# Kernel optimization log

Measured on AMD Instinct MI355X. Metric: run time of the kernel, lower is better.

The kernel has to match this reference:

```python
import jax, jax.numpy as jnp
import numpy as np
from jax import lax

D_MODEL = 512; D_FF = 2048
D_STATE = 16; D_CONV = 4; EXPAND = 2          # mamba_ssm defaults
D_INNER = EXPAND * D_MODEL                    # 1024
DT_RANK = (D_MODEL + 15) // 16                # 32
B, W, C, D = 2, 1024, 64, 8                   # C*D == D_MODEL


def setup_inputs():
    key = jax.random.key(0)
    ks = jax.random.split(key, 24)
    def p(k, shape, s=0.02):
        return jax.random.normal(k, shape, jnp.float32) * s
    inp = {"x": jax.random.normal(ks[0], (B, W, C, D), jnp.float32)}
    for i, pref in enumerate(["fm", "bm"]):
        o = 1 + i * 7
        inp[pref + "_in_W"] = p(ks[o], (2 * D_INNER, D_MODEL))
        inp[pref + "_conv_W"] = p(ks[o + 1], (D_INNER, D_CONV))
        inp[pref + "_conv_b"] = jnp.zeros((D_INNER,), jnp.float32)
        inp[pref + "_xproj_W"] = p(ks[o + 2], (DT_RANK + 2 * D_STATE, D_INNER))
        inp[pref + "_dt_W"] = p(ks[o + 3], (D_INNER, DT_RANK))
        inp[pref + "_dt_b"] = p(ks[o + 4], (D_INNER,), 0.1)
        inp[pref + "_A_log"] = jnp.log(jnp.broadcast_to(
            jnp.arange(1, D_STATE + 1, dtype=jnp.float32), (D_INNER, D_STATE)))
        inp[pref + "_D"] = jnp.ones((D_INNER,), jnp.float32)
        inp[pref + "_out_W"] = p(ks[o + 5], (D_MODEL, D_INNER))
    inp["ln1_g"] = jnp.ones((D_MODEL,), jnp.float32); inp["ln1_b"] = jnp.zeros((D_MODEL,), jnp.float32)
    inp["ln2_g"] = jnp.ones((D_MODEL,), jnp.float32); inp["ln2_b"] = jnp.zeros((D_MODEL,), jnp.float32)
    inp["ln3_g"] = jnp.ones((D_MODEL,), jnp.float32); inp["ln3_b"] = jnp.zeros((D_MODEL,), jnp.float32)
    inp["ff_W1"] = p(ks[15], (D_FF, D_MODEL)); inp["ff_b1"] = jnp.zeros((D_FF,), jnp.float32)
    inp["ff_W2"] = p(ks[16], (D_MODEL, D_FF)); inp["ff_b2"] = jnp.zeros((D_MODEL,), jnp.float32)
    return inp


def _silu(x):
    return x * jax.nn.sigmoid(x)


def _layernorm(x, g, b, eps=1e-5):
    mu = jnp.mean(x, -1, keepdims=True)
    var = jnp.var(x, -1, keepdims=True)
    return (x - mu) * lax.rsqrt(var + eps) * g + b


def _mamba(u, in_W, conv_W, conv_b, xproj_W, dt_W, dt_b, A_log, Dp, out_W):
    # u: (B, L, d_model). Standard Mamba block (mamba_ssm reference math).
    xz = jnp.einsum('bld,ed->ble', u, in_W)            # (B, L, 2*d_inner)
    xm, z = jnp.split(xz, 2, axis=-1)
    # causal depthwise conv along L
    xc = lax.conv_general_dilated(
        xm.transpose(0, 2, 1), conv_W[:, None, :], (1,),
        [(D_CONV - 1, 0)], feature_group_count=D_INNER)
    xm = _silu((xc + conv_b[None, :, None]).transpose(0, 2, 1))  # (B, L, d_inner)
    dbc = jnp.einsum('bld,ed->ble', xm, xproj_W)       # (B, L, dt_rank + 2*d_state)
    dt = dbc[..., :DT_RANK]
    Bm = dbc[..., DT_RANK:DT_RANK + D_STATE]           # (B, L, d_state)
    Cm = dbc[..., DT_RANK + D_STATE:]                  # (B, L, d_state)
    delta = jax.nn.softplus(jnp.einsum('blr,dr->bld', dt, dt_W) + dt_b)  # (B, L, d_inner)
    A = -jnp.exp(A_log)                                # (d_inner, d_state)
    dA = jnp.exp(delta[..., None] * A)                 # (B, L, d_inner, d_state)
    dBu = delta[..., None] * Bm[:, :, None, :] * xm[..., None]

    def step(h, inputs):
        dA_t, dBu_t = inputs
        h = dA_t * h + dBu_t
        return h, h

    h0 = jnp.zeros((u.shape[0], D_INNER, D_STATE), u.dtype)
    _, hs = lax.scan(step, h0, (dA.transpose(1, 0, 2, 3), dBu.transpose(1, 0, 2, 3)))
    y = jnp.einsum('lbds,lbs->bld', hs, Cm.transpose(1, 0, 2))
    y = y + xm * Dp
    y = y * _silu(z)
    return jnp.einsum('ble,de->bld', y, out_W)         # (B, L, d_model)


def reference(x,
              fm_in_W, fm_conv_W, fm_conv_b, fm_xproj_W, fm_dt_W, fm_dt_b, fm_A_log, fm_D, fm_out_W,
              bm_in_W, bm_conv_W, bm_conv_b, bm_xproj_W, bm_dt_W, bm_dt_b, bm_A_log, bm_D, bm_out_W,
              ln1_g, ln1_b, ln2_g, ln2_b, ln3_g, ln3_b,
              ff_W1, ff_b1, ff_W2, ff_b2):
    b, w, c, d = x.shape
    xf = x.reshape(b, w, c * d)
    fwd = _mamba(xf, fm_in_W, fm_conv_W, fm_conv_b, fm_xproj_W, fm_dt_W, fm_dt_b, fm_A_log, fm_D, fm_out_W)
    bwd = jnp.flip(_mamba(jnp.flip(xf, 1), bm_in_W, bm_conv_W, bm_conv_b, bm_xproj_W,
                          bm_dt_W, bm_dt_b, bm_A_log, bm_D, bm_out_W), 1)
    an1 = _layernorm(xf + fwd, ln1_g, ln1_b)   # AddNorm: LN(x + dropout(y)); dropout off at eval
    an2 = _layernorm(xf + bwd, ln2_g, ln2_b)
    out = an1 + an2
    h = jnp.maximum(jnp.einsum('bld,fd->blf', out, ff_W1) + ff_b1, 0)
    ff = jnp.einsum('blf,df->bld', h, ff_W2) + ff_b2
    out = _layernorm(ff + ff, ln3_g, ln3_b)    # an3(out, out) == LN(out + out)
    return out.reshape(b, w, c, d)
```

## Files before the change

kernel.cpp:

```cpp
#include <hip/hip_runtime.h>
#include <hip/hip_bf16.h>
#include <math.h>

#define MM 2048
#define BATCH 2
#define SEQ 1024
#define DMODEL 512
#define DINNER 1024
#define DSTATE 16
#define DTRANK 32
#define DFF 2048

#define NCHUNK 16
#define CHUNK 64
#define GTOT 65536

typedef short bf16x8 __attribute__((ext_vector_type(8)));
typedef float floatx4 __attribute__((ext_vector_type(4)));
typedef unsigned short ushort8v __attribute__((ext_vector_type(8)));
typedef unsigned short ushort4v __attribute__((ext_vector_type(4)));

__device__ __forceinline__ unsigned short f2bf(float f) {
    union { float f; unsigned u; } v; v.f = f;
    unsigned r = v.u + 0x7FFF + ((v.u >> 16) & 1);
    return (unsigned short)(r >> 16);
}
__device__ __forceinline__ float bf2f(unsigned short u) {
    union { unsigned u; float f; } v; v.u = ((unsigned)u) << 16; return v.f;
}

__device__ __forceinline__ float rowsum16(float x) {
    union { float f; int i; } a, b;
    a.f = x;
    b.i = __builtin_amdgcn_update_dpp(0, a.i, 0x128, 0xF, 0xF, false); a.f += b.f;
    b.i = __builtin_amdgcn_update_dpp(0, a.i, 0x124, 0xF, 0xF, false); a.f += b.f;
    b.i = __builtin_amdgcn_update_dpp(0, a.i, 0x122, 0xF, 0xF, false); a.f += b.f;
    b.i = __builtin_amdgcn_update_dpp(0, a.i, 0x121, 0xF, 0xF, false); a.f += b.f;
    return a.f;
}

#define GLOAD_LDS16(gp, lp) __builtin_amdgcn_global_load_lds( \
    (const __attribute__((address_space(1))) unsigned int*)(gp), \
    (__attribute__((address_space(3))) unsigned int*)(lp), 16, 0, 0)


template<int EPI, int OUTBF16>
__global__ __launch_bounds__(256) void gemm_mfma_batch(
    int M, int N, int K,
    const unsigned short* __restrict__ A0, const unsigned short* __restrict__ A1, int lda,
    const unsigned short* __restrict__ B0, const unsigned short* __restrict__ B1, int ldb,
    const float* __restrict__ bias,
    void* __restrict__ C0, void* __restrict__ C1, int ldc)
{
    __shared__ unsigned short As[128 * 32];
    __shared__ unsigned short Bs[128 * 32];
    const int z = blockIdx.z;
    const unsigned short* A = z ? A1 : A0;
    const unsigned short* B = z ? B1 : B0;
    void* Cout = z ? C1 : C0;
    const int tid  = threadIdx.x;
    const int wave = tid >> 6;
    const int lane = tid & 63;
    const int bm = blockIdx.y * 128;
    const int bn = blockIdx.x * 128;

    const int strow = lane & 15;
    const int stkc  = lane >> 4;
    const int wr = wave >> 1, wc = wave & 1;
    const int frow = lane & 15;
    const int fkc  = lane >> 4;

    floatx4 acc[4][4];
    #pragma unroll
    for (int i = 0; i < 4; ++i)
        #pragma unroll
        for (int j = 0; j < 4; ++j)
            acc[i][j] = (floatx4){0.f, 0.f, 0.f, 0.f};

    for (int k0 = 0; k0 < K; k0 += 32) {
        __syncthreads();
        #pragma unroll
        for (int q = 0; q < 2; ++q) {
            int g = wave * 2 + q;
            GLOAD_LDS16(A + (size_t)(bm + g * 16 + strow) * lda + k0 + stkc * 8,
                        As + g * 512);
        }
        #pragma unroll
        for (int q = 0; q < 2; ++q) {
            int g = wave * 2 + q;
            GLOAD_LDS16(B + (size_t)(bn + g * 16 + strow) * ldb + k0 + stkc * 8,
                        Bs + g * 512);
        }
        __syncthreads();

        bf16x8 af[4], bfr[4];
        #pragma unroll
        for (int i = 0; i < 4; ++i)
            af[i] = *(const bf16x8*)(As + (wr * 4 + i) * 512 + fkc * 128 + frow * 8);
        #pragma unroll
        for (int j = 0; j < 4; ++j)
            bfr[j] = *(const bf16x8*)(Bs + (wc * 4 + j) * 512 + fkc * 128 + frow * 8);
        #pragma unroll
        for (int i = 0; i < 4; ++i)
            #pragma unroll
            for (int j = 0; j < 4; ++j)
                acc[i][j] = __builtin_amdgcn_mfma_f32_16x16x32_bf16(
                    af[i], bfr[j], acc[i][j], 0, 0, 0);
    }

    const int orow0 = bm + wr * 64 + (lane >> 4) * 4;
    const int ocol0 = bn + wc * 64 + (lane & 15);
    #pragma unroll
    for (int j = 0; j < 4; ++j) {
        const int col = ocol0 + j * 16;
        const float bv = bias ? bias[col] : 0.f;
        #pragma unroll
        for (int i = 0; i < 4; ++i) {
            #pragma unroll
            for (int r = 0; r < 4; ++r) {
                int row = orow0 + i * 16 + r;
                float t = acc[i][j][r] + bv;
                if (EPI == 1) t = fmaxf(t, 0.f);
                if (OUTBF16)
                    ((unsigned short*)Cout)[(size_t)row * ldc + col] = f2bf(t);
                else
                    ((float*)Cout)[(size_t)row * ldc + col] = t;
            }
        }
    }
}

__global__ __launch_bounds__(256) void gemm_inproj_kernel(
    const unsigned short* __restrict__ A,
    const unsigned short* __restrict__ B0, const unsigned short* __restrict__ B1,
    float* __restrict__ Cx0, float* __restrict__ Cz0,
    float* __restrict__ Cx1, float* __restrict__ Cz1)
{
    __shared__ unsigned short As[128 * 32];
    __shared__ unsigned short Bs[128 * 32];
    const int z = blockIdx.z;
    const unsigned short* B = z ? B1 : B0;
    const int tid  = threadIdx.x;
    const int wave = tid >> 6;
    const int lane = tid & 63;
    const int bm = blockIdx.y * 128;
    const int bn = blockIdx.x * 128;

    const int strow = lane & 15;
    const int stkc  = lane >> 4;
    const int wr = wave >> 1, wc = wave & 1;
    const int frow = lane & 15;
    const int fkc  = lane >> 4;

    floatx4 acc[4][4];
    #pragma unroll
    for (int i = 0; i < 4; ++i)
        #pragma unroll
        for (int j = 0; j < 4; ++j)
            acc[i][j] = (floatx4){0.f, 0.f, 0.f, 0.f};

    for (int k0 = 0; k0 < DMODEL; k0 += 32) {
        __syncthreads();
        #pragma unroll
        for (int q = 0; q < 2; ++q) {
            int g = wave * 2 + q;
            GLOAD_LDS16(A + (size_t)(bm + g * 16 + strow) * DMODEL + k0 + stkc * 8,
                        As + g * 512);
        }
        #pragma unroll
        for (int q = 0; q < 2; ++q) {
            int g = wave * 2 + q;
            GLOAD_LDS16(B + (size_t)(bn + g * 16 + strow) * DMODEL + k0 + stkc * 8,
                        Bs + g * 512);
        }
        __syncthreads();

        bf16x8 af[4], bfr[4];
        #pragma unroll
        for (int i = 0; i < 4; ++i)
            af[i] = *(const bf16x8*)(As + (wr * 4 + i) * 512 + fkc * 128 + frow * 8);
        #pragma unroll
        for (int j = 0; j < 4; ++j)
            bfr[j] = *(const bf16x8*)(Bs + (wc * 4 + j) * 512 + fkc * 128 + frow * 8);
        #pragma unroll
        for (int i = 0; i < 4; ++i)
            #pragma unroll
            for (int j = 0; j < 4; ++j)
                acc[i][j] = __builtin_amdgcn_mfma_f32_16x16x32_bf16(
                    af[i], bfr[j], acc[i][j], 0, 0, 0);
    }

    const int zh = bn >= DINNER;
    float* C = z ? (zh ? Cz1 : Cx1) : (zh ? Cz0 : Cx0);
    const int cb = zh ? DINNER : 0;
    const int orow0 = bm + wr * 64 + (lane >> 4) * 4;
    const int ocol0 = bn + wc * 64 + (lane & 15) - cb;
    #pragma unroll
    for (int j = 0; j < 4; ++j) {
        const int col = ocol0 + j * 16;
        #pragma unroll
        for (int i = 0; i < 4; ++i)
            #pragma unroll
            for (int r = 0; r < 4; ++r)
                C[(size_t)(orow0 + i * 16 + r) * DINNER + col] = acc[i][j][r];
    }
}

template<int NSPLIT>
__global__ __launch_bounds__(256) void gemm_mfma_splitk(
    int M, int N, int K,
    const unsigned short* __restrict__ A0, const unsigned short* __restrict__ A1, int lda,
    const unsigned short* __restrict__ B0, const unsigned short* __restrict__ B1, int ldb,
    float* __restrict__ part, int ldc)
{
    __shared__ unsigned short As[128 * 32];
    __shared__ unsigned short Bs[128 * 32];
    const int z = blockIdx.z;
    const int dir = z / NSPLIT, sp = z % NSPLIT;
    const unsigned short* A = dir ? A1 : A0;
    const unsigned short* B = dir ? B1 : B0;
    float* Cp = part + (size_t)z * M * ldc;
    const int kbeg = sp * (K / NSPLIT);
    const int kend = kbeg + (K / NSPLIT);
    const int tid  = threadIdx.x;
    const int wave = tid >> 6;
    const int lane = tid & 63;
    const int bm = blockIdx.y * 128;
    const int bn = blockIdx.x * 128;

    const int strow = lane & 15;
    const int stkc  = lane >> 4;
    const int wr = wave >> 1, wc = wave & 1;
    const int frow = lane & 15;
    const int fkc  = lane >> 4;

    floatx4 acc[4][4];
    #pragma unroll
    for (int i = 0; i < 4; ++i)
        #pragma unroll
        for (int j = 0; j < 4; ++j)
            acc[i][j] = (floatx4){0.f, 0.f, 0.f, 0.f};

    for (int k0 = kbeg; k0 < kend; k0 += 32) {
        __syncthreads();
        #pragma unroll
        for (int q = 0; q < 2; ++q) {
            int g = wave * 2 + q;
            GLOAD_LDS16(A + (size_t)(bm + g * 16 + strow) * lda + k0 + stkc * 8,
                        As + g * 512);
        }
        #pragma unroll
        for (int q = 0; q < 2; ++q) {
            int g = wave * 2 + q;
            GLOAD_LDS16(B + (size_t)(bn + g * 16 + strow) * ldb + k0 + stkc * 8,
                        Bs + g * 512);
        }
        __syncthreads();

        bf16x8 af[4], bfr[4];
        #pragma unroll
        for (int i = 0; i < 4; ++i)
            af[i] = *(const bf16x8*)(As + (wr * 4 + i) * 512 + fkc * 128 + frow * 8);
        #pragma unroll
        for (int j = 0; j < 4; ++j)
            bfr[j] = *(const bf16x8*)(Bs + (wc * 4 + j) * 512 + fkc * 128 + frow * 8);
        #pragma unroll
        for (int i = 0; i < 4; ++i)
            #pragma unroll
            for (int j = 0; j < 4; ++j)
                acc[i][j] = __builtin_amdgcn_mfma_f32_16x16x32_bf16(
                    af[i], bfr[j], acc[i][j], 0, 0, 0);
    }

    const int orow0 = bm + wr * 64 + (lane >> 4) * 4;
    const int ocol0 = bn + wc * 64 + (lane & 15);
    #pragma unroll
    for (int j = 0; j < 4; ++j) {
        const int col = ocol0 + j * 16;
        #pragma unroll
        for (int i = 0; i < 4; ++i)
            #pragma unroll
            for (int r = 0; r < 4; ++r)
                Cp[(size_t)(orow0 + i * 16 + r) * ldc + col] = acc[i][j][r];
    }
}

__global__ __launch_bounds__(256) void xproj_splitk_kernel(
    const unsigned short* __restrict__ A_f, const unsigned short* __restrict__ A_b,
    const unsigned short* __restrict__ Wf,  const unsigned short* __restrict__ Wb,
    float* __restrict__ part)
{
    __shared__ unsigned short As[128 * 32];
    __shared__ unsigned short Bs[64 * 32];
    const int tid = threadIdx.x, wave = tid >> 6, lane = tid & 63;
    const int bm = blockIdx.x * 128;
    const int dir = blockIdx.y >> 2, sp = blockIdx.y & 3;
    const unsigned short* A = dir ? A_b : A_f;
    const unsigned short* W = dir ? Wb  : Wf;
    float* Cp = part + (size_t)blockIdx.y * MM * 64;
    const int kbeg = sp * 256, kend = kbeg + 256;

    const int strow = lane & 15;
    const int stkc  = lane >> 4;
    const int frow = lane & 15;
    const int fkc  = lane >> 4;

    floatx4 acc[2][4];
    #pragma unroll
    for (int i = 0; i < 2; ++i)
        #pragma unroll
        for (int j = 0; j < 4; ++j)
            acc[i][j] = (floatx4){0.f, 0.f, 0.f, 0.f};

    for (int k0 = kbeg; k0 < kend; k0 += 32) {
        __syncthreads();
        #pragma unroll
        for (int q = 0; q < 2; ++q) {
            int g = wave * 2 + q;
            GLOAD_LDS16(A + (size_t)(bm + g * 16 + strow) * DINNER + k0 + stkc * 8,
                        As + g * 512);
        }
        GLOAD_LDS16(W + (size_t)(wave * 16 + strow) * DINNER + k0 + stkc * 8,
                    Bs + wave * 512);
        __syncthreads();

        bf16x8 af[2], bfr[4];
        #pragma unroll
        for (int i = 0; i < 2; ++i)
            af[i] = *(const bf16x8*)(As + (wave * 2 + i) * 512 + fkc * 128 + frow * 8);
        #pragma unroll
        for (int j = 0; j < 4; ++j)
            bfr[j] = *(const bf16x8*)(Bs + j * 512 + fkc * 128 + frow * 8);
        #pragma unroll
        for (int i = 0; i < 2; ++i)
            #pragma unroll
            for (int j = 0; j < 4; ++j)
                acc[i][j] = __builtin_amdgcn_mfma_f32_16x16x32_bf16(
                    af[i], bfr[j], acc[i][j], 0, 0, 0);
    }

    const int orow0 = bm + wave * 32 + (lane >> 4) * 4;
    #pragma unroll
    for (int j = 0; j < 4; ++j) {
        const int col = (lane & 15) + j * 16;
        #pragma unroll
        for (int i = 0; i < 2; ++i)
            #pragma unroll
            for (int r = 0; r < 4; ++r)
                Cp[(size_t)(orow0 + i * 16 + r) * 64 + col] = acc[i][j][r];
    }
}

__global__ __launch_bounds__(256) void xproj_reduce_kernel(
    const float* __restrict__ part,
    float* __restrict__ dbc_f, float* __restrict__ dbc_b,
    float* __restrict__ bct_f, float* __restrict__ bct_b)
{
    const int dir = blockIdx.y;
    const int i = (blockIdx.x * 256 + threadIdx.x) * 4;
    const float* p = part + (size_t)dir * 4 * (MM * 64);
    float4 a = *(const float4*)(p + i);
    #pragma unroll
    for (int s = 1; s < 4; ++s) {
        float4 t = *(const float4*)(p + (size_t)s * (MM * 64) + i);
        a.x += t.x; a.y += t.y; a.z += t.z; a.w += t.w;
    }
    const int m = i >> 6, c = i & 63;
    if (c < 32) {
        float* dbc = dir ? dbc_b : dbc_f;
        *(float4*)(dbc + (size_t)m * 32 + c) = a;
    } else {
        float* bct = dir ? bct_b : bct_f;
        *(float4*)(bct + (size_t)m * 32 + (c - 32)) = a;
    }
}

__global__ __launch_bounds__(256) void dtproj_batch_kernel(
    int M, int N, int K,
    const float* __restrict__ A0, const float* __restrict__ A1, int lda,
    const float* __restrict__ B0, const float* __restrict__ B1, int ldb,
    const float* __restrict__ bias0, const float* __restrict__ bias1,
    unsigned short* __restrict__ C0, unsigned short* __restrict__ C1, int ldc)
{
    __shared__ float As[16][64];
    __shared__ float Bs[16][64];
    const int z = blockIdx.z;
    const float* A = z ? A1 : A0;
    const float* B = z ? B1 : B0;
    const float* biasR = z ? bias1 : bias0;
    unsigned short* C = z ? C1 : C0;
    const int tid = threadIdx.x;
    const int tx = tid & 15, ty = tid >> 4;
    const int bm = blockIdx.y * 64, bn = blockIdx.x * 64;
    const int lm = tid & 63;
    const int lk = (tid >> 6) * 4;
    const float* Arow = A + (size_t)(bm + lm) * lda + lk;
    const float* Brow = B + (size_t)(bn + lm) * ldb + lk;
    float acc[4][4] = {};
    for (int k0 = 0; k0 < K; k0 += 16) {
        float4 av = *(const float4*)(Arow + k0);
        float4 bv = *(const float4*)(Brow + k0);
        __syncthreads();
        As[lk+0][lm] = av.x; As[lk+1][lm] = av.y; As[lk+2][lm] = av.z; As[lk+3][lm] = av.w;
        Bs[lk+0][lm] = bv.x; Bs[lk+1][lm] = bv.y; Bs[lk+2][lm] = bv.z; Bs[lk+3][lm] = bv.w;
        __syncthreads();
        #pragma unroll
        for (int k = 0; k < 16; ++k) {
            float4 a = *(const float4*)(&As[k][ty*4]);
            float4 b = *(const float4*)(&Bs[k][tx*4]);
            float ar[4] = {a.x,a.y,a.z,a.w};
            float br[4] = {b.x,b.y,b.z,b.w};
            #pragma unroll
            for (int i = 0; i < 4; ++i)
                #pragma unroll
                for (int j = 0; j < 4; ++j)
                    acc[i][j] = fmaf(ar[i], br[j], acc[i][j]);
        }
    }
    const int row0 = bm + ty*4, col0 = bn + tx*4;
    #pragma unroll
    for (int i = 0; i < 4; ++i) {
        float br = biasR[row0 + i];
        ushort4v o;
        #pragma unroll
        for (int j = 0; j < 4; ++j) {
            float t = acc[i][j] + br;
            o[j] = f2bf(fmaxf(t, 0.f) + log1pf(__expf(-fabsf(t))));
        }
        *(ushort4v*)(C + (size_t)(row0 + i) * ldc + col0) = o;
    }
}

__global__ __launch_bounds__(256) void cast_pre_kernel(
    const float* __restrict__ x, const float* __restrict__ w0,
    const float* __restrict__ w1, const float* __restrict__ xp0,
    const float* __restrict__ xp1, unsigned short* __restrict__ dst)
{
    int i = (blockIdx.x * 256 + threadIdx.x) * 8;
    const float* src; int off;
    if      (i < 1048576) { src = x;   off = 0; }
    else if (i < 2097152) { src = w0;  off = 1048576; }
    else if (i < 3145728) { src = w1;  off = 2097152; }
    else if (i < 3211264) { src = xp0; off = 3145728; }
    else                  { src = xp1; off = 3211264; }
    float4 a = *(const float4*)(src + i - off);
    float4 b = *(const float4*)(src + i - off + 4);
    ushort8v o;
    o[0] = f2bf(a.x); o[1] = f2bf(a.y); o[2] = f2bf(a.z); o[3] = f2bf(a.w);
    o[4] = f2bf(b.x); o[5] = f2bf(b.y); o[6] = f2bf(b.z); o[7] = f2bf(b.w);
    *(ushort8v*)(dst + i) = o;
}

__global__ __launch_bounds__(256) void cast_post_kernel(
    const float* __restrict__ w0, const float* __restrict__ w1,
    const float* __restrict__ w2, const float* __restrict__ w3,
    unsigned short* __restrict__ dst)
{
    int i = (blockIdx.x * 256 + threadIdx.x) * 8;
    const float* src; int off;
    if      (i < 524288)  { src = w0; off = 0; }
    else if (i < 1048576) { src = w1; off = 524288; }
    else if (i < 2097152) { src = w2; off = 1048576; }
    else                  { src = w3; off = 2097152; }
    float4 a = *(const float4*)(src + i - off);
    float4 b = *(const float4*)(src + i - off + 4);
    ushort8v o;
    o[0] = f2bf(a.x); o[1] = f2bf(a.y); o[2] = f2bf(a.z); o[3] = f2bf(a.w);
    o[4] = f2bf(b.x); o[5] = f2bf(b.y); o[6] = f2bf(b.z); o[7] = f2bf(b.w);
    *(ushort8v*)(dst + i) = o;
}

__global__ __launch_bounds__(256) void conv_silu_tr_kernel(
    const float* __restrict__ x_f, const float* __restrict__ x_b,
    const float* __restrict__ Wf,  const float* __restrict__ Wb,
    const float* __restrict__ cbf, const float* __restrict__ cbb,
    unsigned short* __restrict__ of,  unsigned short* __restrict__ ob,
    unsigned short* __restrict__ otf, unsigned short* __restrict__ otb)
{
    __shared__ unsigned short t[32][34];
    const int dir = blockIdx.z;
    const float* xo = dir ? x_b : x_f;
    const float* convW = dir ? Wb : Wf;
    const float* convb = dir ? cbb : cbf;
    unsigned short* xm  = dir ? ob : of;
    unsigned short* xmT = dir ? otb : otf;
    const int m0 = blockIdx.x * 32, d0 = blockIdx.y * 32;
    const int tx = threadIdx.x & 31, ty = threadIdx.x >> 5;
    const int d = d0 + tx;
    float4 wv = *(const float4*)(convW + d * 4);
    float w[4] = {wv.x, wv.y, wv.z, wv.w};
    const float cb = convb[d];
    #pragma unroll
    for (int rr = 0; rr < 32; rr += 8) {
        int m = m0 + ty + rr;
        int b = m >> 10, l = m & (SEQ - 1);
        float acc = cb;
        #pragma unroll
        for (int j = 0; j < 4; ++j) {
            int p = dir ? (l + 3 - j) : (l - 3 + j);
            if (p >= 0 && p < SEQ)
                acc = fmaf(xo[(size_t)(b * SEQ + p) * DINNER + d], w[j], acc);
        }
        float sig = 1.f / (1.f + __expf(-acc));
        unsigned short v = f2bf(acc * sig);
        xm[(size_t)m * DINNER + d] = v;
        t[ty + rr][tx] = v;
    }
    __syncthreads();
    #pragma unroll
    for (int rr = 0; rr < 32; rr += 8)
        xmT[(size_t)(d0 + ty + rr) * MM + m0 + tx] = t[tx][ty + rr];
}

template<int DIR>
__device__ __forceinline__ void pass1_body(
    const unsigned short* __restrict__ deltaT, const unsigned short* __restrict__ xmT,
    const float* __restrict__ bct, const float* __restrict__ Alog,
    const float* __restrict__ Dv,
    unsigned short* __restrict__ y0T, float* __restrict__ cumT,
    float* __restrict__ Pout, float* __restrict__ Hout)
{
    const int tid = threadIdx.x;
    const int s = tid & 15;
    const int dloc = tid >> 4;
    const int d = blockIdx.x * 16 + dloc;
    const int b = blockIdx.y / NCHUNK;
    const int c = blockIdx.y % NCHUNK;

    const float A  = -__expf(Alog[d * DSTATE + s]);
    const float Dp = Dv[d];
    const unsigned short* dRow = deltaT + (size_t)d * MM + b * SEQ;
    const unsigned short* xRow = xmT + (size_t)d * MM + b * SEQ;
    const float* bcRow = bct + (size_t)(b * SEQ) * 32 + s;
    unsigned short* yRow = y0T + (size_t)d * MM + b * SEQ;
    float* uRow = cumT + (size_t)d * MM + b * SEQ;

    float h = 0.f, sdl = 0.f;
    const int segBase = DIR ? (SEQ - CHUNK - c * CHUNK) : (c * CHUNK);
    for (int ii = 0; ii < CHUNK; ii += 8) {
        const int off = DIR ? (segBase + (CHUNK - 8) - ii) : (segBase + ii);
        ushort8v dl8 = *(const ushort8v*)(dRow + off);
        ushort8v x8  = *(const ushort8v*)(xRow + off);
        const float* bp = bcRow + (size_t)off * 32;
        float Bv[8], Cv[8];
        #pragma unroll
        for (int u = 0; u < 8; ++u) {
            Bv[u] = bp[u * 32];
            Cv[u] = bp[u * 32 + 16];
        }
        float yv[8], cu[8];
        #pragma unroll
        for (int u = 0; u < 8; ++u) {
            const int t = DIR ? (7 - u) : u;
            float dlv = bf2f(dl8[t]);
            float xv  = bf2f(x8[t]);
            float dA = __expf(dlv * A);
            sdl += dlv;
            h = fmaf(dA, h, dlv * Bv[t] * xv);
            float part = rowsum16(h * Cv[t]);
            yv[t] = fmaf(xv, Dp, part);
            cu[t] = sdl;
        }
        if (s == 0) {
            ushort8v y8;
            #pragma unroll
            for (int u = 0; u < 8; ++u) y8[u] = f2bf(yv[u]);
            *(ushort8v*)(yRow + off) = y8;
            *(float4*)(uRow + off)     = (float4){cu[0], cu[1], cu[2], cu[3]};
            *(float4*)(uRow + off + 4) = (float4){cu[4], cu[5], cu[6], cu[7]};
        }
    }
    const int g = ((DIR * BATCH + b) * DINNER + d) * DSTATE + s;
    Pout[(size_t)c * GTOT + g] = __expf(sdl * A);
    Hout[(size_t)c * GTOT + g] = h;
}

__global__ __launch_bounds__(256) void scan_pass1_kernel(
    const unsigned short* __restrict__ dT_f, const unsigned short* __restrict__ dT_b,
    const unsigned short* __restrict__ xT_f, const unsigned short* __restrict__ xT_b,
    const float* __restrict__ bct_f, const float* __restrict__ bct_b,
    const float* __restrict__ Alog_f, const float* __restrict__ Alog_b,
    const float* __restrict__ D_f, const float* __restrict__ D_b,
    unsigned short* __restrict__ y0T_f, unsigned short* __restrict__ y0T_b,
    float* __restrict__ cumT_f, float* __restrict__ cumT_b,
    float* __restrict__ Pout, float* __restrict__ Hout)
{
    if (blockIdx.z == 0)
        pass1_body<0>(dT_f, xT_f, bct_f, Alog_f, D_f, y0T_f, cumT_f, Pout, Hout);
    else
        pass1_body<1>(dT_b, xT_b, bct_b, Alog_b, D_b, y0T_b, cumT_b, Pout, Hout);
}

__global__ __launch_bounds__(256) void scan_carry_kernel(
    const float* __restrict__ P, const float* __restrict__ H,
    float* __restrict__ carry)
{
    const int g = blockIdx.x * 256 + threadIdx.x;
    float h = 0.f;
    #pragma unroll
    for (int c = 0; c < NCHUNK; ++c) {
        carry[(size_t)c * GTOT + g] = h;
        h = fmaf(P[(size_t)c * GTOT + g], h, H[(size_t)c * GTOT + g]);
    }
}

__global__ __launch_bounds__(256) void scan_correct_kernel(
    const unsigned short* __restrict__ y0T_f, const unsigned short* __restrict__ y0T_b,
    const float* __restrict__ cumT_f, const float* __restrict__ cumT_b,
    const float* __restrict__ bct_f, const float* __restrict__ bct_b,
    const float* __restrict__ Alog_f, const float* __restrict__ Alog_b,
    const float* __restrict__ carry,
    const float* __restrict__ z_f, const float* __restrict__ z_b,
    unsigned short* __restrict__ ybf_f, unsigned short* __restrict__ ybf_b)
{
    __shared__ float Cs[16][33];
    __shared__ float Asm[32][16];
    __shared__ float Cy[32][16];
    __shared__ float t[32][33];

    const int dir = blockIdx.z;
    const unsigned short* y0T = dir ? y0T_b : y0T_f;
    const float* cumT = dir ? cumT_b : cumT_f;
    const float* bct  = dir ? bct_b  : bct_f;
    const float* Alog = dir ? Alog_b : Alog_f;
    const float* zon  = dir ? z_b    : z_f;
    unsigned short* ybf = dir ? ybf_b : ybf_f;

    const int m0 = blockIdx.x * 32, d0 = blockIdx.y * 32;
    const int b = m0 >> 10;
    const int l0 = m0 & (SEQ - 1);
    const int c = dir ? ((SEQ - 1 - l0) >> 6) : (l0 >> 6);

    for (int idx = threadIdx.x; idx < 512; idx += 256) {
        int s1 = idx & 15, ml = idx >> 4;
        Cs[s1][ml] = bct[(size_t)(m0 + ml) * 32 + 16 + s1];
        int dl2 = idx >> 4, s2 = idx & 15;
        Asm[dl2][s2] = -__expf(Alog[(d0 + dl2) * DSTATE + s2]);
        Cy[dl2][s2] = carry[(size_t)c * GTOT
            + ((size_t)(dir * BATCH + b) * DINNER + d0 + dl2) * DSTATE + s2];
    }
    __syncthreads();

    const int tx = threadIdx.x & 31, ty = threadIdx.x >> 5;
    #pragma unroll
    for (int rr = 0; rr < 32; rr += 8) {
        const int dloc = ty + rr;
        const size_t base = (size_t)(d0 + dloc) * MM + m0 + tx;
        float u  = cumT[base];
        float y0 = bf2f(y0T[base]);
        float corr = 0.f;
        #pragma unroll
        for (int s = 0; s < DSTATE; ++s)
            corr = fmaf(Cs[s][tx] * Cy[dloc][s], __expf(Asm[dloc][s] * u), corr);
        t[dloc][tx] = y0 + corr;
    }
    __syncthreads();
    #pragma unroll
    for (int rr = 0; rr < 32; rr += 8) {
        int m = m0 + ty + rr, d = d0 + tx;
        float z = zon[(size_t)m * DINNER + d];
        float sig = 1.f / (1.f + __expf(-z));
        ybf[(size_t)m * DINNER + d] = f2bf(t[tx][ty + rr] * (z * sig));
    }
}

__global__ __launch_bounds__(256) void ln_combine_fused_kernel(
    const float* __restrict__ xf, const float* __restrict__ part,
    const float* __restrict__ g1, const float* __restrict__ b1,
    const float* __restrict__ g2, const float* __restrict__ b2,
    unsigned short* __restrict__ out)
{
    const int m = blockIdx.x;
    const int tid = threadIdx.x;
    const float* xr = xf + (size_t)m * DMODEL;
    const float* p0 = part + (size_t)m * DMODEL;
    const float* p1 = p0 + (size_t)MM * DMODEL;
    const float* p2 = p1 + (size_t)MM * DMODEL;
    const float* p3 = p2 + (size_t)MM * DMODEL;
    float v1a = xr[tid]       + p0[tid]       + p1[tid];
    float v1b = xr[tid + 256] + p0[tid + 256] + p1[tid + 256];
    float v2a = xr[tid]       + p2[tid]       + p3[tid];
    float v2b = xr[tid + 256] + p2[tid + 256] + p3[tid + 256];
    float s1 = v1a + v1b, q1 = v1a*v1a + v1b*v1b;
    float s2 = v2a + v2b, q2 = v2a*v2a + v2b*v2b;
    #pragma unroll
    for (int off = 32; off; off >>= 1) {
        s1 += __shfl_xor(s1, off); q1 += __shfl_xor(q1, off);
        s2 += __shfl_xor(s2, off); q2 += __shfl_xor(q2, off);
    }
    __shared__ float sm[4][4];
    const int w = tid >> 6;
    if ((tid & 63) == 0) { sm[w][0] = s1; sm[w][1] = q1; sm[w][2] = s2; sm[w][3] = q2; }
    __syncthreads();
    s1 = sm[0][0] + sm[1][0] + sm[2][0] + sm[3][0];
    q1 = sm[0][1] + sm[1][1] + sm[2][1] + sm[3][1];
    s2 = sm[0][2] + sm[1][2] + sm[2][2] + sm[3][2];
    q2 = sm[0][3] + sm[1][3] + sm[2][3] + sm[3][3];
    const float inv = 1.f / DMODEL;
    float mu1 = s1 * inv, mu2 = s2 * inv;
    float rs1 = rsqrtf(q1 * inv - mu1 * mu1 + 1e-5f);
    float rs2 = rsqrtf(q2 * inv - mu2 * mu2 + 1e-5f);
    unsigned short* orow = out + (size_t)m * DMODEL;
    orow[tid]       = f2bf((v1a - mu1) * rs1 * g1[tid]       + b1[tid]
                         + (v2a - mu2) * rs2 * g2[tid]       + b2[tid]);
    orow[tid + 256] = f2bf((v1b - mu1) * rs1 * g1[tid + 256] + b1[tid + 256]
                         + (v2b - mu2) * rs2 * g2[tid + 256] + b2[tid + 256]);
}

__global__ __launch_bounds__(256) void ln_final_fused_kernel(
    const float* __restrict__ part, const float* __restrict__ bias,
    const float* __restrict__ g, const float* __restrict__ b,
    float* __restrict__ out)
{
    const int m = blockIdx.x;
    const int tid = threadIdx.x;
    const size_t stride = (size_t)MM * DMODEL;
    const float* p = part + (size_t)m * DMODEL;
    float fa = bias[tid]       + p[tid]       + p[stride + tid]
             + p[2*stride + tid]       + p[3*stride + tid];
    float fb = bias[tid + 256] + p[tid + 256] + p[stride + tid + 256]
             + p[2*stride + tid + 256] + p[3*stride + tid + 256];
    float va = 2.f * fa, vb = 2.f * fb;
    float s = va + vb, q = va*va + vb*vb;
    #pragma unroll
    for (int off = 32; off; off >>= 1) {
        s += __shfl_xor(s, off); q += __shfl_xor(q, off);
    }
    __shared__ float sm[4][2];
    const int w = tid >> 6;
    if ((tid & 63) == 0) { sm[w][0] = s; sm[w][1] = q; }
    __syncthreads();
    s = sm[0][0] + sm[1][0] + sm[2][0] + sm[3][0];
    q = sm[0][1] + sm[1][1] + sm[2][1] + sm[3][1];
    const float inv = 1.f / DMODEL;
    float mu = s * inv;
    float rs = rsqrtf(q * inv - mu * mu + 1e-5f);
    float* orow = out + (size_t)m * DMODEL;
    orow[tid]       = (va - mu) * rs * g[tid]       + b[tid];
    orow[tid + 256] = (vb - mu) * rs * g[tid + 256] + b[tid + 256];
}

extern "C" void kernel_launch(void* const* d_in, const int* in_sizes, int n_in,
                              void* d_out, int out_size, void* d_ws, size_t ws_size,
                              hipStream_t stream)
{
    const float* x         = (const float*)d_in[0];
    const float* fm_in_W   = (const float*)d_in[1];
    const float* fm_conv_W = (const float*)d_in[2];
    const float* fm_conv_b = (const float*)d_in[3];
    const float* fm_xproj_W= (const float*)d_in[4];
    const float* fm_dt_W   = (const float*)d_in[5];
    const float* fm_dt_b   = (const float*)d_in[6];
    const float* fm_A_log  = (const float*)d_in[7];
    const float* fm_D      = (const float*)d_in[8];
    const float* fm_out_W  = (const float*)d_in[9];
    const float* bm_in_W   = (const float*)d_in[10];
    const float* bm_conv_W = (const float*)d_in[11];
    const float* bm_conv_b = (const float*)d_in[12];
    const float* bm_xproj_W= (const float*)d_in[13];
    const float* bm_dt_W   = (const float*)d_in[14];
    const float* bm_dt_b   = (const float*)d_in[15];
    const float* bm_A_log  = (const float*)d_in[16];
    const float* bm_D      = (const float*)d_in[17];
    const float* bm_out_W  = (const float*)d_in[18];
    const float* ln1_g     = (const float*)d_in[19];
    const float* ln1_b     = (const float*)d_in[20];
    const float* ln2_g     = (const float*)d_in[21];
    const float* ln2_b     = (const float*)d_in[22];
    const float* ln3_g     = (const float*)d_in[23];
    const float* ln3_b     = (const float*)d_in[24];
    const float* ff_W1     = (const float*)d_in[25];
    const float* ff_b1     = (const float*)d_in[26];
    const float* ff_W2     = (const float*)d_in[27];
    const float* ff_b2     = (const float*)d_in[28];
    float* out = (float*)d_out;

    float* ws = (float*)d_ws;
    size_t o = 0;
    float* xonly_f = ws + o; o += (size_t)MM * DINNER;
    float* xonly_b = ws + o; o += (size_t)MM * DINNER;
    float* zonly_f = ws + o; o += (size_t)MM * DINNER;
    float* zonly_b = ws + o; o += (size_t)MM * DINNER;
    unsigned short* xm_bf_f = (unsigned short*)(ws + o); o += (size_t)MM * DINNER / 2;
    unsigned short* xm_bf_b = (unsigned short*)(ws + o); o += (size_t)MM * DINNER / 2;
    unsigned short* xmT_f   = (unsigned short*)(ws + o); o += (size_t)MM * DINNER / 2;
    unsigned short* xmT_b   = (unsigned short*)(ws + o); o += (size_t)MM * DINNER / 2;
    unsigned short* deltaT_f= (unsigned short*)(ws + o); o += (size_t)MM * DINNER / 2;
    unsigned short* deltaT_b= (unsigned short*)(ws + o); o += (size_t)MM * DINNER / 2;
    float* dbc_f    = ws + o; o += (size_t)MM * 32;
    float* dbc_b    = ws + o; o += (size_t)MM * 32;
    float* bct_f    = ws + o; o += (size_t)MM * 32;
    float* bct_b    = ws + o; o += (size_t)MM * 32;
    unsigned short* y0T_f = (unsigned short*)(ws + o); o += (size_t)MM * DINNER / 2;
    unsigned short* y0T_b = (unsigned short*)(ws + o); o += (size_t)MM * DINNER / 2;
    float* scanP    = ws + o; o += (size_t)NCHUNK * (GTOT / 16) * 16;
    float* scanH    = ws + o; o += (size_t)NCHUNK * (GTOT / 16) * 16;
    float* scanCy   = ws + o; o += (size_t)NCHUNK * (GTOT / 16) * 16;
    float* gpart    = ws + o; o += (size_t)4 * MM * DMODEL;

    float* cumT_f = xonly_f;
    float* cumT_b = xonly_b;
    unsigned short* x_bf       = (unsigned short*)scanP;
    unsigned short* fm_inW_bf  = x_bf + 1048576;
    unsigned short* bm_inW_bf  = fm_inW_bf + 1048576;
    unsigned short* fm_xpW_bf  = bm_inW_bf + 1048576;
    unsigned short* bm_xpW_bf  = fm_xpW_bf + 65536;
    unsigned short* ybf_f = (unsigned short*)scanP;
    unsigned short* ybf_b = (unsigned short*)scanH;
    unsigned short* fm_outW_bf = (unsigned short*)zonly_f;
    unsigned short* bm_outW_bf = fm_outW_bf + 524288;
    unsigned short* W1_bf      = bm_outW_bf + 524288;
    unsigned short* W2_bf      = W1_bf + 1048576;
    unsigned short* outsum_bf  = (unsigned short*)xonly_b;
    unsigned short* h_bf = (unsigned short*)deltaT_f;

    cast_pre_kernel<<<3276800 / 2048, 256, 0, stream>>>(
        x, fm_in_W, bm_in_W, fm_xproj_W, bm_xproj_W, x_bf);

    gemm_inproj_kernel<<<dim3(2048/128, MM/128, 2), 256, 0, stream>>>(
        x_bf, fm_inW_bf, bm_inW_bf, xonly_f, zonly_f, xonly_b, zonly_b);

    conv_silu_tr_kernel<<<dim3(MM/32, DINNER/32, 2), 256, 0, stream>>>(
        xonly_f, xonly_b, fm_conv_W, bm_conv_W, fm_conv_b, bm_conv_b,
        xm_bf_f, xm_bf_b, xmT_f, xmT_b);

    xproj_splitk_kernel<<<dim3(MM/128, 8), 256, 0, stream>>>(
        xm_bf_f, xm_bf_b, fm_xpW_bf, bm_xpW_bf, gpart);
    xproj_reduce_kernel<<<dim3((MM*64)/1024, 2), 256, 0, stream>>>(
        gpart, dbc_f, dbc_b, bct_f, bct_b);

    dtproj_batch_kernel<<<dim3(MM/64, DINNER/64, 2), 256, 0, stream>>>(
        DINNER, MM, DTRANK, fm_dt_W, bm_dt_W, DTRANK, dbc_f, dbc_b, 32,
        fm_dt_b, bm_dt_b, deltaT_f, deltaT_b, MM);

    scan_pass1_kernel<<<dim3(DINNER/16, BATCH*NCHUNK, 2), 256, 0, stream>>>(
        deltaT_f, deltaT_b, xmT_f, xmT_b, bct_f, bct_b,
        fm_A_log, bm_A_log, fm_D, bm_D,
        y0T_f, y0T_b, cumT_f, cumT_b, scanP, scanH);
    scan_carry_kernel<<<GTOT/256, 256, 0, stream>>>(scanP, scanH, scanCy);
    scan_correct_kernel<<<dim3(MM/32, DINNER/32, 2), 256, 0, stream>>>(
        y0T_f, y0T_b, cumT_f, cumT_b, bct_f, bct_b, fm_A_log, bm_A_log,
        scanCy, zonly_f, zonly_b, ybf_f, ybf_b);

    cast_post_kernel<<<3145728 / 2048, 256, 0, stream>>>(
        fm_out_W, bm_out_W, ff_W1, ff_W2, fm_outW_bf);

    gemm_mfma_splitk<2><<<dim3(DMODEL/128, MM/128, 4), 256, 0, stream>>>(
        MM, DMODEL, DINNER, ybf_f, ybf_b, DINNER, fm_outW_bf, bm_outW_bf, DINNER,
        gpart, DMODEL);

    ln_combine_fused_kernel<<<MM, 256, 0, stream>>>(
        x, gpart, ln1_g, ln1_b, ln2_g, ln2_b, outsum_bf);

    gemm_mfma_batch<1,1><<<dim3(DFF/128, MM/128, 1), 256, 0, stream>>>(
        MM, DFF, DMODEL, outsum_bf, outsum_bf, DMODEL, W1_bf, W1_bf, DMODEL,
        ff_b1, h_bf, h_bf, DFF);

    gemm_mfma_splitk<4><<<dim3(DMODEL/128, MM/128, 4), 256, 0, stream>>>(
        MM, DMODEL, DFF, h_bf, h_bf, DFF, W2_bf, W2_bf, DFF, gpart, DMODEL);

    ln_final_fused_kernel<<<MM, 256, 0, stream>>>(
        gpart, ff_b2, ln3_g, ln3_b, out);
}
```

Measured before the change: 330.9 us.

## Unroll GEMM K loops by 64, pack four SSM states per thread, batch carry loads

All MFMA GEMM kernels now stage two 32-wide K slices into doubled LDS buffers per barrier pair, halving the number of synchronisations per K step at the cost of twice the shared memory. The scan pass1 kernel assigns four state dimensions per thread instead of one, using float4 loads for A, B and C and a two-step DPP quad reduction instead of a 16-lane one, so each block now covers 64 channels. The carry kernel loads all chunk P/H values up front to expose memory parallelism. Risks are lower occupancy from the larger LDS footprint and fewer blocks in the scan launch.

```diff
diff --git a/kernel.cpp b/kernel.cpp
--- a/kernel.cpp
+++ b/kernel.cpp
@@ -29,13 +29,11 @@
     union { unsigned u; float f; } v; v.u = ((unsigned)u) << 16; return v.f;
 }
 
-__device__ __forceinline__ float rowsum16(float x) {
+__device__ __forceinline__ float quadsum4(float x) {
     union { float f; int i; } a, b;
     a.f = x;
-    b.i = __builtin_amdgcn_update_dpp(0, a.i, 0x128, 0xF, 0xF, false); a.f += b.f;
-    b.i = __builtin_amdgcn_update_dpp(0, a.i, 0x124, 0xF, 0xF, false); a.f += b.f;
-    b.i = __builtin_amdgcn_update_dpp(0, a.i, 0x122, 0xF, 0xF, false); a.f += b.f;
-    b.i = __builtin_amdgcn_update_dpp(0, a.i, 0x121, 0xF, 0xF, false); a.f += b.f;
+    b.i = __builtin_amdgcn_update_dpp(0, a.i, 0xB1, 0xF, 0xF, false); a.f += b.f;
+    b.i = __builtin_amdgcn_update_dpp(0, a.i, 0x4E, 0xF, 0xF, false); a.f += b.f;
     return a.f;
 }
 
@@ -52,8 +50,8 @@
     const float* __restrict__ bias,
     void* __restrict__ C0, void* __restrict__ C1, int ldc)
 {
-    __shared__ unsigned short As[128 * 32];
-    __shared__ unsigned short Bs[128 * 32];
+    __shared__ unsigned short As[2][128 * 32];
+    __shared__ unsigned short Bs[2][128 * 32];
     const int z = blockIdx.z;
     const unsigned short* A = z ? A1 : A0;
     const unsigned short* B = z ? B1 : B0;
@@ -77,35 +75,41 @@
         for (int j = 0; j < 4; ++j)
             acc[i][j] = (floatx4){0.f, 0.f, 0.f, 0.f};
 
-    for (int k0 = 0; k0 < K; k0 += 32) {
-        __syncthreads();
-        #pragma unroll
-        for (int q = 0; q < 2; ++q) {
-            int g = wave * 2 + q;
-            GLOAD_LDS16(A + (size_t)(bm + g * 16 + strow) * lda + k0 + stkc * 8,
-                        As + g * 512);
-        }
-        #pragma unroll
-        for (int q = 0; q < 2; ++q) {
-            int g = wave * 2 + q;
-            GLOAD_LDS16(B + (size_t)(bn + g * 16 + strow) * ldb + k0 + stkc * 8,
-                        Bs + g * 512);
-        }
-        __syncthreads();
-
-        bf16x8 af[4], bfr[4];
-        #pragma unroll
-        for (int i = 0; i < 4; ++i)
-            af[i] = *(const bf16x8*)(As + (wr * 4 + i) * 512 + fkc * 128 + frow * 8);
-        #pragma unroll
-        for (int j = 0; j < 4; ++j)
-            bfr[j] = *(const bf16x8*)(Bs + (wc * 4 + j) * 512 + fkc * 128 + frow * 8);
-        #pragma unroll
-        for (int i = 0; i < 4; ++i)
+    for (int k0 = 0; k0 < K; k0 += 64) {
+        __syncthreads();
+        #pragma unroll
+        for (int hh = 0; hh < 2; ++hh) {
+            #pragma unroll
+            for (int q = 0; q < 2; ++q) {
+                int g = wave * 2 + q;
+                GLOAD_LDS16(A + (size_t)(bm + g * 16 + strow) * lda + k0 + hh * 32 + stkc * 8,
+                            As[hh] + g * 512);
+            }
+            #pragma unroll
+            for (int q = 0; q < 2; ++q) {
+                int g = wave * 2 + q;
+                GLOAD_LDS16(B + (size_t)(bn + g * 16 + strow) * ldb + k0 + hh * 32 + stkc * 8,
+                            Bs[hh] + g * 512);
+            }
+        }
+        __syncthreads();
+
+        #pragma unroll
+        for (int hh = 0; hh < 2; ++hh) {
+            bf16x8 af[4], bfr[4];
+            #pragma unroll
+            for (int i = 0; i < 4; ++i)
+                af[i] = *(const bf16x8*)(As[hh] + (wr * 4 + i) * 512 + fkc * 128 + frow * 8);
             #pragma unroll
             for (int j = 0; j < 4; ++j)
-                acc[i][j] = __builtin_amdgcn_mfma_f32_16x16x32_bf16(
-                    af[i], bfr[j], acc[i][j], 0, 0, 0);
+                bfr[j] = *(const bf16x8*)(Bs[hh] + (wc * 4 + j) * 512 + fkc * 128 + frow * 8);
+            #pragma unroll
+            for (int i = 0; i < 4; ++i)
+                #pragma unroll
+                for (int j = 0; j < 4; ++j)
+                    acc[i][j] = __builtin_amdgcn_mfma_f32_16x16x32_bf16(
+                        af[i], bfr[j], acc[i][j], 0, 0, 0);
+        }
     }
 
     const int orow0 = bm + wr * 64 + (lane >> 4) * 4;
@@ -136,8 +140,8 @@
     float* __restrict__ Cx0, float* __restrict__ Cz0,
     float* __restrict__ Cx1, float* __restrict__ Cz1)
 {
-    __shared__ unsigned short As[128 * 32];
-    __shared__ unsigned short Bs[128 * 32];
+    __shared__ unsigned short As[2][128 * 32];
+    __shared__ unsigned short Bs[2][128 * 32];
     const int z = blockIdx.z;
     const unsigned short* B = z ? B1 : B0;
     const int tid  = threadIdx.x;
@@ -159,35 +163,41 @@
         for (int j = 0; j < 4; ++j)
             acc[i][j] = (floatx4){0.f, 0.f, 0.f, 0.f};
 
-    for (int k0 = 0; k0 < DMODEL; k0 += 32) {
-        __syncthreads();
-        #pragma unroll
-        for (int q = 0; q < 2; ++q) {
-            int g = wave * 2 + q;
-            GLOAD_LDS16(A + (size_t)(bm + g * 16 + strow) * DMODEL + k0 + stkc * 8,
-                        As + g * 512);
-        }
-        #pragma unroll
-        for (int q = 0; q < 2; ++q) {
-            int g = wave * 2 + q;
-            GLOAD_LDS16(B + (size_t)(bn + g * 16 + strow) * DMODEL + k0 + stkc * 8,
-                        Bs + g * 512);
-        }
-        __syncthreads();
-
-        bf16x8 af[4], bfr[4];
-        #pragma unroll
-        for (int i = 0; i < 4; ++i)
-            af[i] = *(const bf16x8*)(As + (wr * 4 + i) * 512 + fkc * 128 + frow * 8);
-        #pragma unroll
-        for (int j = 0; j < 4; ++j)
-            bfr[j] = *(const bf16x8*)(Bs + (wc * 4 + j) * 512 + fkc * 128 + frow * 8);
-        #pragma unroll
-        for (int i = 0; i < 4; ++i)
+    for (int k0 = 0; k0 < DMODEL; k0 += 64) {
+        __syncthreads();
+        #pragma unroll
+        for (int hh = 0; hh < 2; ++hh) {
+            #pragma unroll
+            for (int q = 0; q < 2; ++q) {
+                int g = wave * 2 + q;
+                GLOAD_LDS16(A + (size_t)(bm + g * 16 + strow) * DMODEL + k0 + hh * 32 + stkc * 8,
+                            As[hh] + g * 512);
+            }
+            #pragma unroll
+            for (int q = 0; q < 2; ++q) {
+                int g = wave * 2 + q;
+                GLOAD_LDS16(B + (size_t)(bn + g * 16 + strow) * DMODEL + k0 + hh * 32 + stkc * 8,
+                            Bs[hh] + g * 512);
+            }
+        }
+        __syncthreads();
+
+        #pragma unroll
+        for (int hh = 0; hh < 2; ++hh) {
+            bf16x8 af[4], bfr[4];
+            #pragma unroll
+            for (int i = 0; i < 4; ++i)
+                af[i] = *(const bf16x8*)(As[hh] + (wr * 4 + i) * 512 + fkc * 128 + frow * 8);
             #pragma unroll
             for (int j = 0; j < 4; ++j)
-                acc[i][j] = __builtin_amdgcn_mfma_f32_16x16x32_bf16(
-                    af[i], bfr[j], acc[i][j], 0, 0, 0);
+                bfr[j] = *(const bf16x8*)(Bs[hh] + (wc * 4 + j) * 512 + fkc * 128 + frow * 8);
+            #pragma unroll
+            for (int i = 0; i < 4; ++i)
+                #pragma unroll
+                for (int j = 0; j < 4; ++j)
+                    acc[i][j] = __builtin_amdgcn_mfma_f32_16x16x32_bf16(
+                        af[i], bfr[j], acc[i][j], 0, 0, 0);
+        }
     }
 
     const int zh = bn >= DINNER;
@@ -213,8 +223,8 @@
     const unsigned short* __restrict__ B0, const unsigned short* __restrict__ B1, int ldb,
     float* __restrict__ part, int ldc)
 {
-    __shared__ unsigned short As[128 * 32];
-    __shared__ unsigned short Bs[128 * 32];
+    __shared__ unsigned short As[2][128 * 32];
+    __shared__ unsigned short Bs[2][128 * 32];
     const int z = blockIdx.z;
     const int dir = z / NSPLIT, sp = z % NSPLIT;
     const unsigned short* A = dir ? A1 : A0;
@@ -241,35 +251,41 @@
         for (int j = 0; j < 4; ++j)
             acc[i][j] = (floatx4){0.f, 0.f, 0.f, 0.f};
 
-    for (int k0 = kbeg; k0 < kend; k0 += 32) {
-        __syncthreads();
-        #pragma unroll
-        for (int q = 0; q < 2; ++q) {
-            int g = wave * 2 + q;
-            GLOAD_LDS16(A + (size_t)(bm + g * 16 + strow) * lda + k0 + stkc * 8,
-                        As + g * 512);
-        }
-        #pragma unroll
-        for (int q = 0; q < 2; ++q) {
-            int g = wave * 2 + q;
-            GLOAD_LDS16(B + (size_t)(bn + g * 16 + strow) * ldb + k0 + stkc * 8,
-                        Bs + g * 512);
-        }
-        __syncthreads();
-
-        bf16x8 af[4], bfr[4];
-        #pragma unroll
-        for (int i = 0; i < 4; ++i)
-            af[i] = *(const bf16x8*)(As + (wr * 4 + i) * 512 + fkc * 128 + frow * 8);
-        #pragma unroll
-        for (int j = 0; j < 4; ++j)
-            bfr[j] = *(const bf16x8*)(Bs + (wc * 4 + j) * 512 + fkc * 128 + frow * 8);
-        #pragma unroll
-        for (int i = 0; i < 4; ++i)
+    for (int k0 = kbeg; k0 < kend; k0 += 64) {
+        __syncthreads();
+        #pragma unroll
+        for (int hh = 0; hh < 2; ++hh) {
+            #pragma unroll
+            for (int q = 0; q < 2; ++q) {
+                int g = wave * 2 + q;
+                GLOAD_LDS16(A + (size_t)(bm + g * 16 + strow) * lda + k0 + hh * 32 + stkc * 8,
+                            As[hh] + g * 512);
+            }
+            #pragma unroll
+            for (int q = 0; q < 2; ++q) {
+                int g = wave * 2 + q;
+                GLOAD_LDS16(B + (size_t)(bn + g * 16 + strow) * ldb + k0 + hh * 32 + stkc * 8,
+                            Bs[hh] + g * 512);
+            }
+        }
+        __syncthreads();
+
+        #pragma unroll
+        for (int hh = 0; hh < 2; ++hh) {
+            bf16x8 af[4], bfr[4];
+            #pragma unroll
+            for (int i = 0; i < 4; ++i)
+                af[i] = *(const bf16x8*)(As[hh] + (wr * 4 + i) * 512 + fkc * 128 + frow * 8);
             #pragma unroll
             for (int j = 0; j < 4; ++j)
-                acc[i][j] = __builtin_amdgcn_mfma_f32_16x16x32_bf16(
-                    af[i], bfr[j], acc[i][j], 0, 0, 0);
+                bfr[j] = *(const bf16x8*)(Bs[hh] + (wc * 4 + j) * 512 + fkc * 128 + frow * 8);
+            #pragma unroll
+            for (int i = 0; i < 4; ++i)
+                #pragma unroll
+                for (int j = 0; j < 4; ++j)
+                    acc[i][j] = __builtin_amdgcn_mfma_f32_16x16x32_bf16(
+                        af[i], bfr[j], acc[i][j], 0, 0, 0);
+        }
     }
 
     const int orow0 = bm + wr * 64 + (lane >> 4) * 4;
@@ -290,8 +306,8 @@
     const unsigned short* __restrict__ Wf,  const unsigned short* __restrict__ Wb,
     float* __restrict__ part)
 {
-    __shared__ unsigned short As[128 * 32];
-    __shared__ unsigned short Bs[64 * 32];
+    __shared__ unsigned short As[2][128 * 32];
+    __shared__ unsigned short Bs[2][64 * 32];
     const int tid = threadIdx.x, wave = tid >> 6, lane = tid & 63;
     const int bm = blockIdx.x * 128;
     const int dir = blockIdx.y >> 2, sp = blockIdx.y & 3;
@@ -312,31 +328,37 @@
         for (int j = 0; j < 4; ++j)
             acc[i][j] = (floatx4){0.f, 0.f, 0.f, 0.f};
 
-    for (int k0 = kbeg; k0 < kend; k0 += 32) {
-        __syncthreads();
-        #pragma unroll
-        for (int q = 0; q < 2; ++q) {
-            int g = wave * 2 + q;
-            GLOAD_LDS16(A + (size_t)(bm + g * 16 + strow) * DINNER + k0 + stkc * 8,
-                        As + g * 512);
-        }
-        GLOAD_LDS16(W + (size_t)(wave * 16 + strow) * DINNER + k0 + stkc * 8,
-                    Bs + wave * 512);
-        __syncthreads();
-
-        bf16x8 af[2], bfr[4];
-        #pragma unroll
-        for (int i = 0; i < 2; ++i)
-            af[i] = *(const bf16x8*)(As + (wave * 2 + i) * 512 + fkc * 128 + frow * 8);
-        #pragma unroll
-        for (int j = 0; j < 4; ++j)
-            bfr[j] = *(const bf16x8*)(Bs + j * 512 + fkc * 128 + frow * 8);
-        #pragma unroll
-        for (int i = 0; i < 2; ++i)
+    for (int k0 = kbeg; k0 < kend; k0 += 64) {
+        __syncthreads();
+        #pragma unroll
+        for (int hh = 0; hh < 2; ++hh) {
+            #pragma unroll
+            for (int q = 0; q < 2; ++q) {
+                int g = wave * 2 + q;
+                GLOAD_LDS16(A + (size_t)(bm + g * 16 + strow) * DINNER + k0 + hh * 32 + stkc * 8,
+                            As[hh] + g * 512);
+            }
+            GLOAD_LDS16(W + (size_t)(wave * 16 + strow) * DINNER + k0 + hh * 32 + stkc * 8,
+                        Bs[hh] + wave * 512);
+        }
+        __syncthreads();
+
+        #pragma unroll
+        for (int hh = 0; hh < 2; ++hh) {
+            bf16x8 af[2], bfr[4];
+            #pragma unroll
+            for (int i = 0; i < 2; ++i)
+                af[i] = *(const bf16x8*)(As[hh] + (wave * 2 + i) * 512 + fkc * 128 + frow * 8);
             #pragma unroll
             for (int j = 0; j < 4; ++j)
-                acc[i][j] = __builtin_amdgcn_mfma_f32_16x16x32_bf16(
-                    af[i], bfr[j], acc[i][j], 0, 0, 0);
+                bfr[j] = *(const bf16x8*)(Bs[hh] + j * 512 + fkc * 128 + frow * 8);
+            #pragma unroll
+            for (int i = 0; i < 2; ++i)
+                #pragma unroll
+                for (int j = 0; j < 4; ++j)
+                    acc[i][j] = __builtin_amdgcn_mfma_f32_16x16x32_bf16(
+                        af[i], bfr[j], acc[i][j], 0, 0, 0);
+        }
     }
 
     const int orow0 = bm + wave * 32 + (lane >> 4) * 4;
@@ -521,47 +543,48 @@
     float* __restrict__ Pout, float* __restrict__ Hout)
 {
     const int tid = threadIdx.x;
-    const int s = tid & 15;
-    const int dloc = tid >> 4;
-    const int d = blockIdx.x * 16 + dloc;
+    const int sq = tid & 3;
+    const int dloc = tid >> 2;
+    const int d = blockIdx.x * 64 + dloc;
     const int b = blockIdx.y / NCHUNK;
     const int c = blockIdx.y % NCHUNK;
 
-    const float A  = -__expf(Alog[d * DSTATE + s]);
+    float4 Av = *(const float4*)(Alog + d * DSTATE + sq * 4);
+    const float A0 = -__expf(Av.x), A1 = -__expf(Av.y);
+    const float A2 = -__expf(Av.z), A3 = -__expf(Av.w);
     const float Dp = Dv[d];
     const unsigned short* dRow = deltaT + (size_t)d * MM + b * SEQ;
     const unsigned short* xRow = xmT + (size_t)d * MM + b * SEQ;
-    const float* bcRow = bct + (size_t)(b * SEQ) * 32 + s;
+    const float* bcRow = bct + (size_t)(b * SEQ) * 32 + sq * 4;
     unsigned short* yRow = y0T + (size_t)d * MM + b * SEQ;
     float* uRow = cumT + (size_t)d * MM + b * SEQ;
 
-    float h = 0.f, sdl = 0.f;
+    float h0 = 0.f, h1 = 0.f, h2 = 0.f, h3 = 0.f, sdl = 0.f;
     const int segBase = DIR ? (SEQ - CHUNK - c * CHUNK) : (c * CHUNK);
     for (int ii = 0; ii < CHUNK; ii += 8) {
         const int off = DIR ? (segBase + (CHUNK - 8) - ii) : (segBase + ii);
         ushort8v dl8 = *(const ushort8v*)(dRow + off);
         ushort8v x8  = *(const ushort8v*)(xRow + off);
-        const float* bp = bcRow + (size_t)off * 32;
-        float Bv[8], Cv[8];
-        #pragma unroll
-        for (int u = 0; u < 8; ++u) {
-            Bv[u] = bp[u * 32];
-            Cv[u] = bp[u * 32 + 16];
-        }
         float yv[8], cu[8];
         #pragma unroll
         for (int u = 0; u < 8; ++u) {
             const int t = DIR ? (7 - u) : u;
+            float4 Bv = *(const float4*)(bcRow + (size_t)(off + t) * 32);
+            float4 Cv = *(const float4*)(bcRow + (size_t)(off + t) * 32 + 16);
             float dlv = bf2f(dl8[t]);
             float xv  = bf2f(x8[t]);
-            float dA = __expf(dlv * A);
             sdl += dlv;
-            h = fmaf(dA, h, dlv * Bv[t] * xv);
-            float part = rowsum16(h * Cv[t]);
+            float dx = dlv * xv;
+            h0 = fmaf(__expf(dlv * A0), h0, dx * Bv.x);
+            h1 = fmaf(__expf(dlv * A1), h1, dx * Bv.y);
+            h2 = fmaf(__expf(dlv * A2), h2, dx * Bv.z);
+            h3 = fmaf(__expf(dlv * A3), h3, dx * Bv.w);
+            float part = h0 * Cv.x + h1 * Cv.y + h2 * Cv.z + h3 * Cv.w;
+            part = quadsum4(part);
             yv[t] = fmaf(xv, Dp, part);
             cu[t] = sdl;
         }
-        if (s == 0) {
+        if (sq == 0) {
             ushort8v y8;
             #pragma unroll
             for (int u = 0; u < 8; ++u) y8[u] = f2bf(yv[u]);
@@ -570,9 +593,10 @@
             *(float4*)(uRow + off + 4) = (float4){cu[4], cu[5], cu[6], cu[7]};
         }
     }
-    const int g = ((DIR * BATCH + b) * DINNER + d) * DSTATE + s;
-    Pout[(size_t)c * GTOT + g] = __expf(sdl * A);
-    Hout[(size_t)c * GTOT + g] = h;
+    const size_t g4 = ((size_t)(DIR * BATCH + b) * DINNER + d) * DSTATE + sq * 4;
+    *(float4*)(Pout + (size_t)c * GTOT + g4) =
+        (float4){__expf(sdl * A0), __expf(sdl * A1), __expf(sdl * A2), __expf(sdl * A3)};
+    *(float4*)(Hout + (size_t)c * GTOT + g4) = (float4){h0, h1, h2, h3};
 }
 
 __global__ __launch_bounds__(256) void scan_pass1_kernel(
@@ -596,11 +620,17 @@
     float* __restrict__ carry)
 {
     const int g = blockIdx.x * 256 + threadIdx.x;
+    float p[NCHUNK], hh[NCHUNK];
+    #pragma unroll
+    for (int c = 0; c < NCHUNK; ++c) {
+        p[c]  = P[(size_t)c * GTOT + g];
+        hh[c] = H[(size_t)c * GTOT + g];
+    }
     float h = 0.f;
     #pragma unroll
     for (int c = 0; c < NCHUNK; ++c) {
         carry[(size_t)c * GTOT + g] = h;
-        h = fmaf(P[(size_t)c * GTOT + g], h, H[(size_t)c * GTOT + g]);
+        h = fmaf(p[c], h, hh[c]);
     }
 }
 
@@ -833,7 +863,7 @@
         DINNER, MM, DTRANK, fm_dt_W, bm_dt_W, DTRANK, dbc_f, dbc_b, 32,
         fm_dt_b, bm_dt_b, deltaT_f, deltaT_b, MM);
 
-    scan_pass1_kernel<<<dim3(DINNER/16, BATCH*NCHUNK, 2), 256, 0, stream>>>(
+    scan_pass1_kernel<<<dim3(DINNER/64, BATCH*NCHUNK, 2), 256, 0, stream>>>(
         deltaT_f, deltaT_b, xmT_f, xmT_b, bct_f, bct_b,
         fm_A_log, bm_A_log, fm_D, bm_D,
         y0T_f, y0T_b, cumT_f, cumT_b, scanP, scanH);
```

After: 305.5 us. 1.08x faster.
